# Kernel tuning notes

Hardware: AMD Instinct MI355X
Metric: run time of the kernel (lower is better)

## Reference

```python
import jax, jax.numpy as jnp
import numpy as np

H = 128   # LSTM hidden size
T = 120   # sequence length
F = 4     # input features


def setup_inputs() -> dict:
    key = jax.random.key(0)
    ks = jax.random.split(key, 11)
    B = 4096
    return {
        "x": jax.random.normal(ks[0], (B, T, F), dtype=jnp.float32),
        "h0": jax.random.uniform(ks[1], (B, H), dtype=jnp.float32),
        "c0": jax.random.uniform(ks[2], (B, H), dtype=jnp.float32),
        "W_ih": jax.random.normal(ks[3], (4 * H, F), dtype=jnp.float32) * 0.05,
        "W_hh": jax.random.normal(ks[4], (4 * H, H), dtype=jnp.float32) * 0.05,
        "b_ih": jax.random.normal(ks[5], (4 * H,), dtype=jnp.float32) * 0.05,
        "b_hh": jax.random.normal(ks[6], (4 * H,), dtype=jnp.float32) * 0.05,
        "fc1_w": jax.random.normal(ks[7], (100, T * H), dtype=jnp.float32) * 0.01,
        "fc1_b": jax.random.normal(ks[8], (100,), dtype=jnp.float32) * 0.01,
        "fc2_w": jax.random.normal(ks[9], (10, 100), dtype=jnp.float32) * 0.1,
        "fc2_b": jax.random.normal(ks[10], (10,), dtype=jnp.float32) * 0.1,
    }


def _lstm(x, h0, c0, W_ih, W_hh, b_ih, b_hh):
    # Precompute input-dependent part of the gates for all timesteps at once.
    # PyTorch gate order: i, f, g, o.  gates_x: [T, B, 4H]
    gates_x = jnp.einsum('btf,gf->tbg', x, W_ih) + b_ih + b_hh

    def step(carry, gx):
        h, c = carry
        g = gx + h @ W_hh.T                      # [B, 4H]
        i = jax.nn.sigmoid(g[:, 0 * H:1 * H])
        f = jax.nn.sigmoid(g[:, 1 * H:2 * H])
        gg = jnp.tanh(g[:, 2 * H:3 * H])
        o = jax.nn.sigmoid(g[:, 3 * H:4 * H])
        c = f * c + i * gg
        h = o * jnp.tanh(c)
        return (h, c), h

    (_, _), hs = jax.lax.scan(step, (h0, c0), gates_x)  # hs: [T, B, H]
    return hs


def reference(x, h0, c0, W_ih, W_hh, b_ih, b_hh, fc1_w, fc1_b, fc2_w, fc2_b):
    B = x.shape[0]
    hs = _lstm(x, h0, c0, W_ih, W_hh, b_ih, b_hh)        # [T, B, H]
    feat = hs.transpose(1, 0, 2).reshape(B, T * H)        # [B, T*H]
    hid = jax.nn.relu(feat @ fc1_w.T + fc1_b)             # [B, 100]
    logits = hid @ fc2_w.T + fc2_b                        # [B, 10]
    return jax.nn.log_softmax(logits, axis=-1)
```

## Files before the change

kernel.cpp:

```cpp
#include <hip/hip_runtime.h>

#define T_LEN 120
#define H 128
#define ROWS 16
#define XSTR 484
#define FC1_STRIDE 15360

#define OFF_WHH   0u
#define OFF_WXB   131072u
#define OFF_FC1W  163840u
#define OFF_FC1B  4096000u

typedef short short8 __attribute__((ext_vector_type(8)));
typedef float f32x4 __attribute__((ext_vector_type(4)));

#define L2E 1.4426950408889634f
#define SWZ(r) (((((r) & 7) ^ (((r) >> 3) << 1))) << 4)

__device__ __forceinline__ unsigned short f2bu(float f) {
  unsigned u = __builtin_bit_cast(unsigned, f);
  u += 0x7fffu + ((u >> 16) & 1u);
  return (unsigned short)(u >> 16);
}
__device__ __forceinline__ float gate_scale(int row) {
  return ((row >> 7) == 2) ? 2.0f * L2E : -L2E;
}

__global__ void prep_all(const float* __restrict__ W_ih, const float* __restrict__ W_hh,
                         const float* __restrict__ b_ih, const float* __restrict__ b_hh,
                         const float* __restrict__ fc1_w, const float* __restrict__ fc1_b,
                         unsigned char* __restrict__ ws) {
  if (blockIdx.x < 1024) {
    unsigned short* w = (unsigned short*)(ws + OFF_FC1W);
    int j = blockIdx.x >> 3;
    int c0 = ((blockIdx.x & 7) * 256 + threadIdx.x) * 8;
    if (c0 >= FC1_STRIDE) return;
    short8 v = {0, 0, 0, 0, 0, 0, 0, 0};
    if (j < 100) {
      const float* src = fc1_w + j * FC1_STRIDE + c0;
#pragma unroll
      for (int e = 0; e < 8; ++e) ((unsigned short*)&v)[e] = f2bu(src[e]);
    }
    *(short8*)(w + j * FC1_STRIDE + c0) = v;
  } else {
    unsigned short* whh = (unsigned short*)(ws + OFF_WHH);
    unsigned short* wxb = (unsigned short*)(ws + OFF_WXB);
    float* fb = (float*)(ws + OFF_FC1B);
    int tid = (blockIdx.x - 1024) * 256 + threadIdx.x;
    const int nt = 8 * 256;
    for (int i = tid; i < 512 * 128; i += nt) {
      int row = i >> 7;
      whh[i] = f2bu(W_hh[i] * gate_scale(row));
    }
    for (int i = tid; i < 512 * 32; i += nt) {
      int j = i >> 5, k = i & 31;
      float s = gate_scale(j);
      float v = 0.f;
      if (k < 4) v = W_ih[j * 4 + k] * s;
      else if (k == 4) v = (b_ih[j] + b_hh[j]) * s;
      wxb[i] = f2bu(v);
    }
    for (int i = tid; i < 128; i += nt) fb[i] = (i < 100) ? fc1_b[i] : 0.f;
  }
}

__global__ __launch_bounds__(512, 2)
void lstm_fused(const float* __restrict__ x, const float* __restrict__ h0,
                const float* __restrict__ c0, const float* __restrict__ fc2_w,
                const float* __restrict__ fc2_b, const unsigned char* __restrict__ ws,
                float* __restrict__ out) {
  __shared__ float x_stage[ROWS * XSTR];
  __shared__ __align__(16) unsigned char h_lds[2 * ROWS * 256];
  __shared__ __align__(16) float fc2w_s[1000];
  __shared__ float fc2b_s[10];
  __shared__ float logit_s[ROWS * 12];

  const int tid = threadIdx.x;
  const int w = tid >> 6;
  const int l = tid & 63;
  const int lq = l >> 4;
  const int lc = l & 15;
  const int r0 = blockIdx.x * ROWS;
  const int hcol = w * 16 + lc;

  const unsigned short* Whh = (const unsigned short*)(ws + OFF_WHH);
  const unsigned short* Wxb = (const unsigned short*)(ws + OFF_WXB);
  const unsigned short* FC1 = (const unsigned short*)(ws + OFF_FC1W);
  const float* FC1B = (const float*)(ws + OFF_FC1B);

  for (int i = tid; i < ROWS * 480; i += 512) {
    int r = i / 480;
    int cc = i - r * 480;
    x_stage[r * XSTR + cc] = x[(r0 + r) * 480 + cc];
  }
  for (int e = tid * 2; e < ROWS * H; e += 1024) {
    int r = e >> 7, c = e & 127;
    unsigned u = (unsigned)f2bu(h0[(r0 + r) * H + c]) |
                 ((unsigned)f2bu(h0[(r0 + r) * H + c + 1]) << 16);
    *(unsigned*)(h_lds + 4096 + r * 256 + ((2 * c) ^ SWZ(r))) = u;
  }
  float c_reg[4];
#pragma unroll
  for (int q = 0; q < 4; ++q) c_reg[q] = c0[(r0 + lq * 4 + q) * H + hcol];

  short8 bhh[4][4], bxb[4];
#pragma unroll
  for (int g = 0; g < 4; ++g) {
    int n0 = (g * 8 + w) * 16;
#pragma unroll
    for (int kk = 0; kk < 4; ++kk)
      bhh[g][kk] = *(const short8*)(Whh + (n0 + lc) * H + kk * 32 + lq * 8);
    bxb[g] = *(const short8*)(Wxb + (n0 + lc) * 32 + lq * 8);
  }
  const unsigned short* fc1row = FC1 + (w * 16 + lc) * FC1_STRIDE;
  f32x4 facc = {0.f, 0.f, 0.f, 0.f};

  __syncthreads();

  short8 ha[4];
#pragma unroll
  for (int kk = 0; kk < 4; ++kk)
    ha[kk] = *(const short8*)(h_lds + 4096 + lc * 256 + ((kk * 64 + lq * 16) ^ SWZ(lc)));

  short8 xa = {0, 0, 0, 0, 0, 0, 0, 0};
  if (lq == 0) {
    const float* xr = &x_stage[lc * XSTR];
    xa[0] = (short)f2bu(xr[0]); xa[1] = (short)f2bu(xr[1]);
    xa[2] = (short)f2bu(xr[2]); xa[3] = (short)f2bu(xr[3]);
    xa[4] = (short)0x3f80;
  }

  const f32x4 zero4 = {0.f, 0.f, 0.f, 0.f};
  f32x4 accX0 = __builtin_amdgcn_mfma_f32_16x16x32_bf16(xa, bxb[0], zero4, 0, 0, 0);
  f32x4 accX1 = __builtin_amdgcn_mfma_f32_16x16x32_bf16(xa, bxb[1], zero4, 0, 0, 0);
  f32x4 accX2 = __builtin_amdgcn_mfma_f32_16x16x32_bf16(xa, bxb[2], zero4, 0, 0, 0);
  f32x4 accX3 = __builtin_amdgcn_mfma_f32_16x16x32_bf16(xa, bxb[3], zero4, 0, 0, 0);

  for (int t = 0; t < T_LEN; ++t) {
    const unsigned short* fp = fc1row + t * 128 + lq * 8;
    short8 fb0 = *(const short8*)(fp + 0);
    short8 fb1 = *(const short8*)(fp + 32);
    short8 fb2 = *(const short8*)(fp + 64);
    short8 fb3 = *(const short8*)(fp + 96);

    f32x4 acc0 = accX0, acc1 = accX1, acc2 = accX2, acc3 = accX3;
#pragma unroll
    for (int kk = 0; kk < 4; ++kk) {
      acc0 = __builtin_amdgcn_mfma_f32_16x16x32_bf16(ha[kk], bhh[0][kk], acc0, 0, 0, 0);
      acc1 = __builtin_amdgcn_mfma_f32_16x16x32_bf16(ha[kk], bhh[1][kk], acc1, 0, 0, 0);
      acc2 = __builtin_amdgcn_mfma_f32_16x16x32_bf16(ha[kk], bhh[2][kk], acc2, 0, 0, 0);
      acc3 = __builtin_amdgcn_mfma_f32_16x16x32_bf16(ha[kk], bhh[3][kk], acc3, 0, 0, 0);
    }

    if (t + 1 < T_LEN && lq == 0) {
      const float* xr = &x_stage[lc * XSTR + (t + 1) * 4];
      xa[0] = (short)f2bu(xr[0]); xa[1] = (short)f2bu(xr[1]);
      xa[2] = (short)f2bu(xr[2]); xa[3] = (short)f2bu(xr[3]);
    }
    accX0 = __builtin_amdgcn_mfma_f32_16x16x32_bf16(xa, bxb[0], zero4, 0, 0, 0);
    accX1 = __builtin_amdgcn_mfma_f32_16x16x32_bf16(xa, bxb[1], zero4, 0, 0, 0);
    accX2 = __builtin_amdgcn_mfma_f32_16x16x32_bf16(xa, bxb[2], zero4, 0, 0, 0);
    accX3 = __builtin_amdgcn_mfma_f32_16x16x32_bf16(xa, bxb[3], zero4, 0, 0, 0);

    float hval[4];
#pragma unroll
    for (int q = 0; q < 4; ++q) {
      float ea = __builtin_amdgcn_exp2f(acc0[q]);
      float eb = __builtin_amdgcn_exp2f(acc1[q]);
      float ec = __builtin_amdgcn_exp2f(acc2[q]);
      float ed = __builtin_amdgcn_exp2f(acc3[q]);
      float a = 1.f + ea, b = 1.f + eb, d = 1.f + ec, e = 1.f + ed;
      float rab = __builtin_amdgcn_rcpf(a * b);
      float rde = __builtin_amdgcn_rcpf(d * e);
      float iv = b * rab;
      float fv = a * rab;
      float gv = 1.f - 2.f * (e * rde);
      float ov = d * rde;
      float cn = fv * c_reg[q] + iv * gv;
      c_reg[q] = cn;
      float et = __builtin_amdgcn_exp2f(2.8853900817779268f * cn);
      hval[q] = ov * (1.f - 2.f * __builtin_amdgcn_rcpf(1.f + et));
    }

    unsigned char* hw = h_lds + (t & 1) * 4096;
#pragma unroll
    for (int q = 0; q < 4; ++q) {
      int r = lq * 4 + q;
      *(unsigned short*)(hw + r * 256 + ((2 * hcol) ^ SWZ(r))) = f2bu(hval[q]);
    }

    asm volatile("s_waitcnt lgkmcnt(0)" ::: "memory");
    __builtin_amdgcn_s_barrier();
    asm volatile("" ::: "memory");

#pragma unroll
    for (int kk = 0; kk < 4; ++kk)
      ha[kk] = *(const short8*)(hw + lc * 256 + ((kk * 64 + lq * 16) ^ SWZ(lc)));
    facc = __builtin_amdgcn_mfma_f32_16x16x32_bf16(ha[0], fb0, facc, 0, 0, 0);
    facc = __builtin_amdgcn_mfma_f32_16x16x32_bf16(ha[1], fb1, facc, 0, 0, 0);
    facc = __builtin_amdgcn_mfma_f32_16x16x32_bf16(ha[2], fb2, facc, 0, 0, 0);
    facc = __builtin_amdgcn_mfma_f32_16x16x32_bf16(ha[3], fb3, facc, 0, 0, 0);
  }

  for (int i = tid; i < 1000; i += 512) fc2w_s[i] = fc2_w[i];
  if (tid < 10) fc2b_s[tid] = fc2_b[tid];
  float bias = FC1B[hcol];
  __syncthreads();
  float* hid = x_stage;
#pragma unroll
  for (int q = 0; q < 4; ++q) {
    float v = facc[q] + bias;
    hid[(lq * 4 + q) * 132 + hcol] = v > 0.f ? v : 0.f;
  }
  __syncthreads();
  if (tid < 160) {
    int r = tid & 15, k = tid >> 4;
    float a = fc2b_s[k];
#pragma unroll 4
    for (int j = 0; j < 100; ++j) a += hid[r * 132 + j] * fc2w_s[k * 100 + j];
    logit_s[r * 12 + k] = a;
  }
  __syncthreads();
  if (tid < 16) {
    int r = tid;
    float m = logit_s[r * 12];
#pragma unroll
    for (int k = 1; k < 10; ++k) m = fmaxf(m, logit_s[r * 12 + k]);
    float s = 0.f;
#pragma unroll
    for (int k = 0; k < 10; ++k)
      s += __builtin_amdgcn_exp2f(L2E * (logit_s[r * 12 + k] - m));
    float ls = __builtin_amdgcn_logf(s) * 0.6931471805599453f;
#pragma unroll
    for (int k = 0; k < 10; ++k)
      out[(r0 + r) * 10 + k] = logit_s[r * 12 + k] - m - ls;
  }
}

extern "C" void kernel_launch(void* const* d_in, const int* in_sizes, int n_in,
                              void* d_out, int out_size, void* d_ws, size_t ws_size,
                              hipStream_t stream) {
  const float* x     = (const float*)d_in[0];
  const float* h0    = (const float*)d_in[1];
  const float* c0    = (const float*)d_in[2];
  const float* W_ih  = (const float*)d_in[3];
  const float* W_hh  = (const float*)d_in[4];
  const float* b_ih  = (const float*)d_in[5];
  const float* b_hh  = (const float*)d_in[6];
  const float* fc1_w = (const float*)d_in[7];
  const float* fc1_b = (const float*)d_in[8];
  const float* fc2_w = (const float*)d_in[9];
  const float* fc2_b = (const float*)d_in[10];
  float* out = (float*)d_out;
  unsigned char* ws = (unsigned char*)d_ws;

  prep_all<<<1032, 256, 0, stream>>>(W_ih, W_hh, b_ih, b_hh, fc1_w, fc1_b, ws);
  lstm_fused<<<256, 512, 0, stream>>>(x, h0, c0, fc2_w, fc2_b, ws, out);
}
```

Before: 151.0 us.

## Halve rows per block to 8 and launch 512 blocks with padded MFMA rows

Each block now processes 8 batch rows instead of 16, and the grid doubles to 512 blocks so every compute unit of the 256-CU device gets work. The 16-row MFMA tile is kept, with real rows mapped to positions 0-1 of each 4-row group and the other rows zero-padded, so half the MFMA work is wasted. The serial 120-step recurrence per block is unchanged, so the intent is to spread work across more CUs at the cost of redundant matrix work, more total weight loads into registers, and doubled FC1 weight traffic.

```diff
diff --git a/kernel.cpp b/kernel.cpp
--- a/kernel.cpp
+++ b/kernel.cpp
@@ -2,7 +2,7 @@
 
 #define T_LEN 120
 #define H 128
-#define ROWS 16
+#define ROWS 8
 #define XSTR 484
 #define FC1_STRIDE 15360
 
@@ -64,13 +64,13 @@
   }
 }
 
-__global__ __launch_bounds__(512, 2)
+__global__ __launch_bounds__(512, 4)
 void lstm_fused(const float* __restrict__ x, const float* __restrict__ h0,
                 const float* __restrict__ c0, const float* __restrict__ fc2_w,
                 const float* __restrict__ fc2_b, const unsigned char* __restrict__ ws,
                 float* __restrict__ out) {
   __shared__ float x_stage[ROWS * XSTR];
-  __shared__ __align__(16) unsigned char h_lds[2 * ROWS * 256];
+  __shared__ __align__(16) unsigned char h_lds[2 * 16 * 256];
   __shared__ __align__(16) float fc2w_s[1000];
   __shared__ float fc2b_s[10];
   __shared__ float logit_s[ROWS * 12];
@@ -88,20 +88,26 @@
   const unsigned short* FC1 = (const unsigned short*)(ws + OFF_FC1W);
   const float* FC1B = (const float*)(ws + OFF_FC1B);
 
+  for (int i = tid; i < 2048; i += 512) {
+    int r = (i >> 6) & 15;
+    if ((r & 3) >= 2) ((unsigned*)h_lds)[i] = 0u;
+  }
   for (int i = tid; i < ROWS * 480; i += 512) {
     int r = i / 480;
     int cc = i - r * 480;
     x_stage[r * XSTR + cc] = x[(r0 + r) * 480 + cc];
   }
-  for (int e = tid * 2; e < ROWS * H; e += 1024) {
-    int r = e >> 7, c = e & 127;
-    unsigned u = (unsigned)f2bu(h0[(r0 + r) * H + c]) |
-                 ((unsigned)f2bu(h0[(r0 + r) * H + c + 1]) << 16);
-    *(unsigned*)(h_lds + 4096 + r * 256 + ((2 * c) ^ SWZ(r))) = u;
-  }
-  float c_reg[4];
-#pragma unroll
-  for (int q = 0; q < 4; ++q) c_reg[q] = c0[(r0 + lq * 4 + q) * H + hcol];
+  {
+    int e = tid * 2;
+    int j = e >> 7, c = e & 127;
+    int tr = ((j >> 1) << 2) + (j & 1);
+    unsigned u = (unsigned)f2bu(h0[(r0 + j) * H + c]) |
+                 ((unsigned)f2bu(h0[(r0 + j) * H + c + 1]) << 16);
+    *(unsigned*)(h_lds + 4096 + tr * 256 + ((2 * c) ^ SWZ(tr))) = u;
+  }
+  float c_reg[2];
+#pragma unroll
+  for (int q = 0; q < 2; ++q) c_reg[q] = c0[(r0 + lq * 2 + q) * H + hcol];
 
   short8 bhh[4][4], bxb[4];
 #pragma unroll
@@ -122,9 +128,11 @@
   for (int kk = 0; kk < 4; ++kk)
     ha[kk] = *(const short8*)(h_lds + 4096 + lc * 256 + ((kk * 64 + lq * 16) ^ SWZ(lc)));
 
+  const int xrow = ((lc >> 2) << 1) + (lc & 1);
+  const bool xreal = ((lc & 3) < 2);
   short8 xa = {0, 0, 0, 0, 0, 0, 0, 0};
-  if (lq == 0) {
-    const float* xr = &x_stage[lc * XSTR];
+  if (lq == 0 && xreal) {
+    const float* xr = &x_stage[xrow * XSTR];
     xa[0] = (short)f2bu(xr[0]); xa[1] = (short)f2bu(xr[1]);
     xa[2] = (short)f2bu(xr[2]); xa[3] = (short)f2bu(xr[3]);
     xa[4] = (short)0x3f80;
@@ -152,8 +160,8 @@
       acc3 = __builtin_amdgcn_mfma_f32_16x16x32_bf16(ha[kk], bhh[3][kk], acc3, 0, 0, 0);
     }
 
-    if (t + 1 < T_LEN && lq == 0) {
-      const float* xr = &x_stage[lc * XSTR + (t + 1) * 4];
+    if (t + 1 < T_LEN && lq == 0 && xreal) {
+      const float* xr = &x_stage[xrow * XSTR + (t + 1) * 4];
       xa[0] = (short)f2bu(xr[0]); xa[1] = (short)f2bu(xr[1]);
       xa[2] = (short)f2bu(xr[2]); xa[3] = (short)f2bu(xr[3]);
     }
@@ -162,9 +170,9 @@
     accX2 = __builtin_amdgcn_mfma_f32_16x16x32_bf16(xa, bxb[2], zero4, 0, 0, 0);
     accX3 = __builtin_amdgcn_mfma_f32_16x16x32_bf16(xa, bxb[3], zero4, 0, 0, 0);
 
-    float hval[4];
-#pragma unroll
-    for (int q = 0; q < 4; ++q) {
+    float hval[2];
+#pragma unroll
+    for (int q = 0; q < 2; ++q) {
       float ea = __builtin_amdgcn_exp2f(acc0[q]);
       float eb = __builtin_amdgcn_exp2f(acc1[q]);
       float ec = __builtin_amdgcn_exp2f(acc2[q]);
@@ -184,7 +192,7 @@
 
     unsigned char* hw = h_lds + (t & 1) * 4096;
 #pragma unroll
-    for (int q = 0; q < 4; ++q) {
+    for (int q = 0; q < 2; ++q) {
       int r = lq * 4 + q;
       *(unsigned short*)(hw + r * 256 + ((2 * hcol) ^ SWZ(r))) = f2bu(hval[q]);
     }
@@ -208,20 +216,20 @@
   __syncthreads();
   float* hid = x_stage;
 #pragma unroll
-  for (int q = 0; q < 4; ++q) {
+  for (int q = 0; q < 2; ++q) {
     float v = facc[q] + bias;
-    hid[(lq * 4 + q) * 132 + hcol] = v > 0.f ? v : 0.f;
-  }
-  __syncthreads();
-  if (tid < 160) {
-    int r = tid & 15, k = tid >> 4;
+    hid[(lq * 2 + q) * 132 + hcol] = v > 0.f ? v : 0.f;
+  }
+  __syncthreads();
+  if (tid < 80) {
+    int r = tid & 7, k = tid >> 3;
     float a = fc2b_s[k];
 #pragma unroll 4
     for (int j = 0; j < 100; ++j) a += hid[r * 132 + j] * fc2w_s[k * 100 + j];
     logit_s[r * 12 + k] = a;
   }
   __syncthreads();
-  if (tid < 16) {
+  if (tid < ROWS) {
     int r = tid;
     float m = logit_s[r * 12];
 #pragma unroll
@@ -255,5 +263,5 @@
   unsigned char* ws = (unsigned char*)d_ws;
 
   prep_all<<<1032, 256, 0, stream>>>(W_ih, W_hh, b_ih, b_hh, fc1_w, fc1_b, ws);
-  lstm_fused<<<256, 512, 0, stream>>>(x, h0, c0, fc2_w, fc2_b, ws, out);
-}
+  lstm_fused<<<512, 512, 0, stream>>>(x, h0, c0, fc2_w, fc2_b, ws, out);
+}
```

Result: slower. 463.4 us (+206.8%).

## Prepack x as bf16 MFMA fragments in LDS and reschedule the LSTM step

Applied to the files above, without the earlier changes.

Converts x to bf16 once during staging, packed per timestep into ready-made MFMA A-fragments with the bias-one column, so the loop loads one short8 instead of doing per-step conversions on a subset of lanes. The recurrent MFMAs now issue first under raised wave priority, and the fc1 weight loads, the next x fragment and the next input-gate MFMAs are moved after the activation math so they overlap with it. The activation math is paired across two rows so one reciprocal serves two values, and the fc2 weight staging moves before the loop. Sharing reciprocals across products may lose a little precision or overflow when the gate exponentials are large.

```diff
diff --git a/kernel.cpp b/kernel.cpp
--- a/kernel.cpp
+++ b/kernel.cpp
@@ -3,7 +3,6 @@
 #define T_LEN 120
 #define H 128
 #define ROWS 16
-#define XSTR 484
 #define FC1_STRIDE 15360
 
 #define OFF_WHH   0u
@@ -13,9 +12,14 @@
 
 typedef short short8 __attribute__((ext_vector_type(8)));
 typedef float f32x4 __attribute__((ext_vector_type(4)));
+typedef unsigned int ui32x4 __attribute__((ext_vector_type(4)));
 
 #define L2E 1.4426950408889634f
 #define SWZ(r) (((((r) & 7) ^ (((r) >> 3) << 1))) << 4)
+#define MFMA __builtin_amdgcn_mfma_f32_16x16x32_bf16
+#define BAR() do { asm volatile("s_waitcnt lgkmcnt(0)" ::: "memory"); \
+                   __builtin_amdgcn_s_barrier(); \
+                   asm volatile("" ::: "memory"); } while (0)
 
 __device__ __forceinline__ unsigned short f2bu(float f) {
   unsigned u = __builtin_bit_cast(unsigned, f);
@@ -69,8 +73,8 @@
                 const float* __restrict__ c0, const float* __restrict__ fc2_w,
                 const float* __restrict__ fc2_b, const unsigned char* __restrict__ ws,
                 float* __restrict__ out) {
-  __shared__ float x_stage[ROWS * XSTR];
-  __shared__ __align__(16) unsigned char h_lds[2 * ROWS * 256];
+  __shared__ __align__(16) unsigned char xab[T_LEN * 256];
+  __shared__ __align__(16) unsigned char h_lds[2 * 4096];
   __shared__ __align__(16) float fc2w_s[1000];
   __shared__ float fc2b_s[10];
   __shared__ float logit_s[ROWS * 12];
@@ -88,10 +92,16 @@
   const unsigned short* FC1 = (const unsigned short*)(ws + OFF_FC1W);
   const float* FC1B = (const float*)(ws + OFF_FC1B);
 
-  for (int i = tid; i < ROWS * 480; i += 512) {
-    int r = i / 480;
-    int cc = i - r * 480;
-    x_stage[r * XSTR + cc] = x[(r0 + r) * 480 + cc];
+  for (int i = tid; i < 1000; i += 512) fc2w_s[i] = fc2_w[i];
+  if (tid < 10) fc2b_s[tid] = fc2_b[tid];
+
+  for (int i = tid; i < ROWS * T_LEN; i += 512) {
+    int rr = i / T_LEN, t = i - rr * T_LEN;
+    f32x4 xv = *(const f32x4*)(x + (r0 + rr) * (T_LEN * 4) + t * 4);
+    unsigned w0 = (unsigned)f2bu(xv[0]) | ((unsigned)f2bu(xv[1]) << 16);
+    unsigned w1 = (unsigned)f2bu(xv[2]) | ((unsigned)f2bu(xv[3]) << 16);
+    ui32x4 pk = {w0, w1, 0x3f80u, 0u};
+    *(ui32x4*)(xab + t * 256 + rr * 16) = pk;
   }
   for (int e = tid * 2; e < ROWS * H; e += 1024) {
     int r = e >> 7, c = e & 127;
@@ -121,92 +131,86 @@
 #pragma unroll
   for (int kk = 0; kk < 4; ++kk)
     ha[kk] = *(const short8*)(h_lds + 4096 + lc * 256 + ((kk * 64 + lq * 16) ^ SWZ(lc)));
-
-  short8 xa = {0, 0, 0, 0, 0, 0, 0, 0};
-  if (lq == 0) {
-    const float* xr = &x_stage[lc * XSTR];
-    xa[0] = (short)f2bu(xr[0]); xa[1] = (short)f2bu(xr[1]);
-    xa[2] = (short)f2bu(xr[2]); xa[3] = (short)f2bu(xr[3]);
-    xa[4] = (short)0x3f80;
-  }
+  short8 xa = *(const short8*)(xab + lc * 16);
 
   const f32x4 zero4 = {0.f, 0.f, 0.f, 0.f};
-  f32x4 accX0 = __builtin_amdgcn_mfma_f32_16x16x32_bf16(xa, bxb[0], zero4, 0, 0, 0);
-  f32x4 accX1 = __builtin_amdgcn_mfma_f32_16x16x32_bf16(xa, bxb[1], zero4, 0, 0, 0);
-  f32x4 accX2 = __builtin_amdgcn_mfma_f32_16x16x32_bf16(xa, bxb[2], zero4, 0, 0, 0);
-  f32x4 accX3 = __builtin_amdgcn_mfma_f32_16x16x32_bf16(xa, bxb[3], zero4, 0, 0, 0);
+  f32x4 accX0 = MFMA(xa, bxb[0], zero4, 0, 0, 0);
+  f32x4 accX1 = MFMA(xa, bxb[1], zero4, 0, 0, 0);
+  f32x4 accX2 = MFMA(xa, bxb[2], zero4, 0, 0, 0);
+  f32x4 accX3 = MFMA(xa, bxb[3], zero4, 0, 0, 0);
 
   for (int t = 0; t < T_LEN; ++t) {
+    __builtin_amdgcn_s_setprio(1);
+    f32x4 acc0 = accX0, acc1 = accX1, acc2 = accX2, acc3 = accX3;
+#pragma unroll
+    for (int kk = 0; kk < 4; ++kk) {
+      acc0 = MFMA(ha[kk], bhh[0][kk], acc0, 0, 0, 0);
+      acc1 = MFMA(ha[kk], bhh[1][kk], acc1, 0, 0, 0);
+      acc2 = MFMA(ha[kk], bhh[2][kk], acc2, 0, 0, 0);
+      acc3 = MFMA(ha[kk], bhh[3][kk], acc3, 0, 0, 0);
+    }
+
     const unsigned short* fp = fc1row + t * 128 + lq * 8;
     short8 fb0 = *(const short8*)(fp + 0);
     short8 fb1 = *(const short8*)(fp + 32);
     short8 fb2 = *(const short8*)(fp + 64);
     short8 fb3 = *(const short8*)(fp + 96);
-
-    f32x4 acc0 = accX0, acc1 = accX1, acc2 = accX2, acc3 = accX3;
-#pragma unroll
-    for (int kk = 0; kk < 4; ++kk) {
-      acc0 = __builtin_amdgcn_mfma_f32_16x16x32_bf16(ha[kk], bhh[0][kk], acc0, 0, 0, 0);
-      acc1 = __builtin_amdgcn_mfma_f32_16x16x32_bf16(ha[kk], bhh[1][kk], acc1, 0, 0, 0);
-      acc2 = __builtin_amdgcn_mfma_f32_16x16x32_bf16(ha[kk], bhh[2][kk], acc2, 0, 0, 0);
-      acc3 = __builtin_amdgcn_mfma_f32_16x16x32_bf16(ha[kk], bhh[3][kk], acc3, 0, 0, 0);
-    }
-
-    if (t + 1 < T_LEN && lq == 0) {
-      const float* xr = &x_stage[lc * XSTR + (t + 1) * 4];
-      xa[0] = (short)f2bu(xr[0]); xa[1] = (short)f2bu(xr[1]);
-      xa[2] = (short)f2bu(xr[2]); xa[3] = (short)f2bu(xr[3]);
-    }
-    accX0 = __builtin_amdgcn_mfma_f32_16x16x32_bf16(xa, bxb[0], zero4, 0, 0, 0);
-    accX1 = __builtin_amdgcn_mfma_f32_16x16x32_bf16(xa, bxb[1], zero4, 0, 0, 0);
-    accX2 = __builtin_amdgcn_mfma_f32_16x16x32_bf16(xa, bxb[2], zero4, 0, 0, 0);
-    accX3 = __builtin_amdgcn_mfma_f32_16x16x32_bf16(xa, bxb[3], zero4, 0, 0, 0);
-
-    float hval[4];
-#pragma unroll
-    for (int q = 0; q < 4; ++q) {
-      float ea = __builtin_amdgcn_exp2f(acc0[q]);
-      float eb = __builtin_amdgcn_exp2f(acc1[q]);
-      float ec = __builtin_amdgcn_exp2f(acc2[q]);
-      float ed = __builtin_amdgcn_exp2f(acc3[q]);
-      float a = 1.f + ea, b = 1.f + eb, d = 1.f + ec, e = 1.f + ed;
-      float rab = __builtin_amdgcn_rcpf(a * b);
-      float rde = __builtin_amdgcn_rcpf(d * e);
-      float iv = b * rab;
-      float fv = a * rab;
-      float gv = 1.f - 2.f * (e * rde);
-      float ov = d * rde;
-      float cn = fv * c_reg[q] + iv * gv;
-      c_reg[q] = cn;
-      float et = __builtin_amdgcn_exp2f(2.8853900817779268f * cn);
-      hval[q] = ov * (1.f - 2.f * __builtin_amdgcn_rcpf(1.f + et));
-    }
+    int tn = (t + 1 < T_LEN) ? t + 1 : t;
+    short8 xan = *(const short8*)(xab + tn * 256 + lc * 16);
 
     unsigned char* hw = h_lds + (t & 1) * 4096;
 #pragma unroll
-    for (int q = 0; q < 4; ++q) {
-      int r = lq * 4 + q;
-      *(unsigned short*)(hw + r * 256 + ((2 * hcol) ^ SWZ(r))) = f2bu(hval[q]);
-    }
-
-    asm volatile("s_waitcnt lgkmcnt(0)" ::: "memory");
-    __builtin_amdgcn_s_barrier();
-    asm volatile("" ::: "memory");
+    for (int qp = 0; qp < 2; ++qp) {
+      const int q0 = qp * 2, q1 = q0 + 1;
+      float ea0 = __builtin_amdgcn_exp2f(acc0[q0]), ea1 = __builtin_amdgcn_exp2f(acc0[q1]);
+      float eb0 = __builtin_amdgcn_exp2f(acc1[q0]), eb1 = __builtin_amdgcn_exp2f(acc1[q1]);
+      float ec0 = __builtin_amdgcn_exp2f(acc2[q0]), ec1 = __builtin_amdgcn_exp2f(acc2[q1]);
+      float ed0 = __builtin_amdgcn_exp2f(acc3[q0]), ed1 = __builtin_amdgcn_exp2f(acc3[q1]);
+      float a0 = 1.f + ea0, b0 = 1.f + eb0, d0 = 1.f + ec0, e0 = 1.f + ed0;
+      float a1 = 1.f + ea1, b1 = 1.f + eb1, d1 = 1.f + ec1, e1 = 1.f + ed1;
+      float ab0 = a0 * b0, ab1 = a1 * b1, de0 = d0 * e0, de1 = d1 * e1;
+      float rAB = __builtin_amdgcn_rcpf(ab0 * ab1);
+      float rDE = __builtin_amdgcn_rcpf(de0 * de1);
+      float rab0 = rAB * ab1, rab1 = rAB * ab0;
+      float rde0 = rDE * de1, rde1 = rDE * de0;
+      float iv0 = b0 * rab0, fv0 = a0 * rab0;
+      float iv1 = b1 * rab1, fv1 = a1 * rab1;
+      float gv0 = 1.f - 2.f * (e0 * rde0), ov0 = d0 * rde0;
+      float gv1 = 1.f - 2.f * (e1 * rde1), ov1 = d1 * rde1;
+      float cn0 = fv0 * c_reg[q0] + iv0 * gv0;
+      float cn1 = fv1 * c_reg[q1] + iv1 * gv1;
+      c_reg[q0] = cn0; c_reg[q1] = cn1;
+      float et0 = __builtin_amdgcn_exp2f(2.8853900817779268f * cn0);
+      float et1 = __builtin_amdgcn_exp2f(2.8853900817779268f * cn1);
+      float t0 = 1.f + et0, t1 = 1.f + et1;
+      float rT = __builtin_amdgcn_rcpf(t0 * t1);
+      float hv0 = ov0 * (1.f - 2.f * (rT * t1));
+      float hv1 = ov1 * (1.f - 2.f * (rT * t0));
+      int r0r = lq * 4 + q0, r1r = lq * 4 + q1;
+      *(unsigned short*)(hw + r0r * 256 + ((2 * hcol) ^ SWZ(r0r))) = f2bu(hv0);
+      *(unsigned short*)(hw + r1r * 256 + ((2 * hcol) ^ SWZ(r1r))) = f2bu(hv1);
+    }
+    __builtin_amdgcn_s_setprio(0);
+
+    accX0 = MFMA(xan, bxb[0], zero4, 0, 0, 0);
+    accX1 = MFMA(xan, bxb[1], zero4, 0, 0, 0);
+    accX2 = MFMA(xan, bxb[2], zero4, 0, 0, 0);
+    accX3 = MFMA(xan, bxb[3], zero4, 0, 0, 0);
+
+    BAR();
 
 #pragma unroll
     for (int kk = 0; kk < 4; ++kk)
       ha[kk] = *(const short8*)(hw + lc * 256 + ((kk * 64 + lq * 16) ^ SWZ(lc)));
-    facc = __builtin_amdgcn_mfma_f32_16x16x32_bf16(ha[0], fb0, facc, 0, 0, 0);
-    facc = __builtin_amdgcn_mfma_f32_16x16x32_bf16(ha[1], fb1, facc, 0, 0, 0);
-    facc = __builtin_amdgcn_mfma_f32_16x16x32_bf16(ha[2], fb2, facc, 0, 0, 0);
-    facc = __builtin_amdgcn_mfma_f32_16x16x32_bf16(ha[3], fb3, facc, 0, 0, 0);
-  }
-
-  for (int i = tid; i < 1000; i += 512) fc2w_s[i] = fc2_w[i];
-  if (tid < 10) fc2b_s[tid] = fc2_b[tid];
+    facc = MFMA(ha[0], fb0, facc, 0, 0, 0);
+    facc = MFMA(ha[1], fb1, facc, 0, 0, 0);
+    facc = MFMA(ha[2], fb2, facc, 0, 0, 0);
+    facc = MFMA(ha[3], fb3, facc, 0, 0, 0);
+  }
+
   float bias = FC1B[hcol];
   __syncthreads();
-  float* hid = x_stage;
+  float* hid = (float*)xab;
 #pragma unroll
   for (int q = 0; q < 4; ++q) {
     float v = facc[q] + bias;
```

Result: faster. 147.2 us (-2.5%).
